# Kernel tuning notes

Measured on AMD Instinct MI355X. Metric: run time of the kernel, lower is better.

Reference implementation:

```python
import jax, jax.numpy as jnp
import numpy as np

B, T, C, L = 128, 1024, 128, 128
EPS = 1e-7        # keras.backend.epsilon()
NEG = -1e30       # log-space -inf surrogate


def setup_inputs() -> dict:
    key = jax.random.key(0)
    k1, k2, k3, k4 = jax.random.split(key, 4)
    logits = jax.random.normal(k1, (B, T, C), dtype=jnp.float32)
    y_pred = jax.nn.softmax(logits, axis=-1)                      # ctc_batch_cost expects probs
    y_true = jax.random.randint(k2, (B, L), 0, C - 1)             # blank = C-1 excluded from labels
    input_len = jax.random.randint(k3, (B, 1), T // 2, T + 1)
    label_len = jax.random.randint(k4, (B, 1), L // 2, L + 1)
    return {"y_true": y_true, "y_pred": y_pred, "input_len": input_len, "label_len": label_len}


def _ctc_loss(y_pred, y_true, input_len, label_len):
    # Faithful port of keras ctc_batch_cost: blank index = C-1, merge repeated,
    # log(y_pred + eps), returns per-sample loss with shape [B, 1].
    log_probs = jnp.log(y_pred + EPS)                             # [B,T,C]
    b, t_max, c = log_probs.shape
    blank = c - 1
    l = y_true.shape[1]
    s = 2 * l + 1
    # extended label sequence: blank, l1, blank, l2, ..., blank   [B,S]
    ext = jnp.full((b, s), blank, dtype=y_true.dtype).at[:, 1::2].set(y_true)
    # emission log-prob of each extended symbol at each frame     [B,T,S]
    lp_ext = jnp.take_along_axis(
        log_probs, jnp.broadcast_to(ext[:, None, :], (b, t_max, s)), axis=2)
    # skip transition s-2 -> s allowed iff ext[s] != blank and ext[s] != ext[s-2]
    allow_skip = jnp.concatenate(
        [jnp.zeros((b, 2), bool), (ext[:, 2:] != blank) & (ext[:, 2:] != ext[:, :-2])], axis=1)
    alpha0 = jnp.full((b, s), NEG, dtype=log_probs.dtype).at[:, 0].set(0.0)
    in_len = input_len.reshape(b, 1).astype(jnp.int32)

    def step(alpha, xt):
        lp_t, t = xt                                              # lp_t: [B,S]
        a1 = jnp.pad(alpha[:, :-1], ((0, 0), (1, 0)), constant_values=NEG)
        a2 = jnp.where(allow_skip,
                       jnp.pad(alpha[:, :-2], ((0, 0), (2, 0)), constant_values=NEG), NEG)
        new = lp_t + jnp.logaddexp(jnp.logaddexp(alpha, a1), a2)
        new = jnp.where(t < in_len, new, alpha)                   # freeze past input_len
        return new, None

    alpha, _ = jax.lax.scan(step, alpha0, (jnp.swapaxes(lp_ext, 0, 1), jnp.arange(t_max)))
    lab = label_len.reshape(b, 1).astype(jnp.int32)
    a_last = jnp.take_along_axis(alpha, 2 * lab, axis=1)          # ends at final blank
    a_prev = jnp.take_along_axis(alpha, jnp.maximum(2 * lab - 1, 0), axis=1)  # or final label
    return -jnp.logaddexp(a_last, a_prev)                         # [B,1]


def reference(y_true, y_pred, input_len, label_len):
    return _ctc_loss(y_pred, y_true, input_len, label_len)
```

## Files before the change

kernel.cpp:

```cpp
#include <hip/hip_runtime.h>
#include <cstdint>

#define NB 128
#define NT 1024
#define NC 128
#define NL 128
#define NS 257
#define EPSF 1e-7f
#define LN2F 0.69314718055994530942f
#define NEGL2 -1.442695e30f

__device__ __forceinline__ float fexp2(float x){ return __builtin_amdgcn_exp2f(x); }
__device__ __forceinline__ float flog2(float x){ return __builtin_amdgcn_logf(x); }

__device__ __forceinline__ float shup1(float x){
    int r = __builtin_amdgcn_update_dpp(0, __float_as_int(x), 0x138, 0xf, 0xf, true);
    return __int_as_float(r);
}
__device__ __forceinline__ int shup1i(int x){
    return __builtin_amdgcn_update_dpp(0, x, 0x138, 0xf, 0xf, true);
}

__device__ __forceinline__ void dma16(const float* g, float* lds){
    __builtin_amdgcn_global_load_lds((const __attribute__((address_space(1))) void*)g,
                                     (__attribute__((address_space(3))) void*)lds,
                                     16, 0, 0);
}

#define VM_DRAIN() asm volatile("s_waitcnt vmcnt(0)" ::: "memory")

#define FENCE12(S) asm volatile("" \
  : "+v"(S##B[0]),"+v"(S##B[1]),"+v"(S##B[2]),"+v"(S##B[3]), \
    "+v"(S##A[0]),"+v"(S##A[1]),"+v"(S##A[2]),"+v"(S##A[3]), \
    "+v"(S##C[0]),"+v"(S##C[1]),"+v"(S##C[2]),"+v"(S##C[3]))

#define FILL(S, gg) do{ _Pragma("unroll") \
    for (int r_ = 0; r_ < 4; ++r_){ \
        S##B[r_] = lB[((gg)*4 + r_) * NC]; \
        S##A[r_] = lA[((gg)*4 + r_) * NC]; \
        S##C[r_] = lC[((gg)*4 + r_) * NC]; } }while(0)

#define GROUP(S, gg) do{ _Pragma("unroll") \
    for (int r_ = 0; r_ < 4; ++r_){ \
        const bool commit_ = !freeze || ((k*32 + (gg)*4 + r_) < Tn); \
        step1(S##B[r_], S##A[r_], S##C[r_], commit_); \
        if (r_ < 3) shm3 = shup1(m3); } \
    boundary(early); }while(0)

__global__ __launch_bounds__(64,1)
void ctc_fwd_kernel(const int* __restrict__ y_true,
                    const float* __restrict__ y_pred,
                    const int* __restrict__ input_len,
                    const int* __restrict__ label_len,
                    float* __restrict__ out)
{
    __shared__ float buf[2][32 * NC];
    __shared__ float lg_alpha[NS + 3];

    const int b    = blockIdx.x;
    const int lane = threadIdx.x;
    const float* __restrict__ base = y_pred + (size_t)b * NT * NC;

    int Tn = input_len[b];
    Tn = Tn < 0 ? 0 : (Tn > NT ? NT : Tn);

    const int* __restrict__ yrow = y_true + b * NL;
    const int y0v = yrow[2 * lane]     & (NC - 1);
    const int y1v = yrow[2 * lane + 1] & (NC - 1);
    const int yp  = shup1i(y1v);
    const bool skip1 = (lane > 0) && (y0v != yp);
    const bool skip3 = (y1v != y0v);
    const bool isl0  = (lane == 0);
    const bool isl63 = (lane == 63);

    float m0 = isl0 ? 1.f : 0.f, m1 = 0.f, m2 = 0.f, m3 = 0.f, m4 = 0.f;
    float e   = 0.f;
    float f0  = isl0 ? 0.f : 1.f;
    float fs1 = skip1 ? f0 : 0.f;
    float shm3 = 0.f;

    float s0B[4], s0A[4], s0C[4], s1B[4], s1A[4], s1C[4];

    auto dma_chunk = [&](int c){
        const float* gsrc = base + (size_t)c * 32 * NC;
        float* dst = &buf[c & 1][0];
        #pragma unroll
        for (int i = 0; i < 16; ++i)
            dma16(gsrc + i * 256 + lane * 4, dst + i * 256);
    };

    auto step1 = [&](float Pb, float Pa, float Pc, bool commit){
        Pb += EPSF; Pa += EPSF; Pc += EPSF;
        float t3  = skip3 ? m1 : 0.f;
        float n3  = Pc * ((m3 + m2) + t3);
        float n2  = Pb * (m2 + m1);
        float n4  = Pb * (m4 + m3);
        float pm1 = shm3 * f0;
        float t1  = shm3 * fs1;
        float n0  = Pb * (m0 + pm1);
        float n1  = Pa * ((m1 + m0) + t1);
        if (commit) { m0 = n0; m1 = n1; m2 = n2; m3 = n3; m4 = n4; }
    };

    auto boundary = [&](bool early){
        float mx = fmaxf(fmaxf(m0, m1), fmaxf(m2, m3));
        if (isl63) mx = fmaxf(mx, m4);
        const uint32_t bx = __float_as_uint(mx);
        const uint32_t eb = bx >> 23;
        const float inv = __uint_as_float((254u - eb) << 23);
        const float ef  = (float)((int)eb - 127);
        const bool dead = (mx == 0.f);
        if (early) {
            float e1 = dead ? e : (e + ef);
            float s1 = shup1(e1);
            float e2 = (dead && !isl0) ? s1 : e1;
            float s2 = shup1(e2);
            e = (dead && !isl0) ? s2 : e2;
            float d = fminf(fmaxf(s2 - e, -126.f), 126.f);
            f0 = isl0 ? 0.f : fexp2(d);
        } else {
            e = dead ? e : (e + ef);
            float s1 = shup1(e);
            float d = fminf(fmaxf(s1 - e, -126.f), 126.f);
            f0 = isl0 ? 0.f : fexp2(d);
        }
        fs1 = skip1 ? f0 : 0.f;
        m0 *= inv; m1 *= inv; m2 *= inv; m3 *= inv; m4 *= inv;
        shm3 = shup1(m3);
    };

    auto chunkbody = [&](int k, bool early, bool freeze){
        const int h = k & 1;
        const float* lB = &buf[h][NC - 1];
        const float* lA = &buf[h][y0v];
        const float* lC = &buf[h][y1v];

        FILL(s0, 0);
        if (k + 1 < 32) dma_chunk(k + 1);

        FILL(s1, 1); FENCE12(s0); GROUP(s0, 0);
        FILL(s0, 2); FENCE12(s1); GROUP(s1, 1);
        FILL(s1, 3); FENCE12(s0); GROUP(s0, 2);
        FILL(s0, 4); FENCE12(s1); GROUP(s1, 3);
        FILL(s1, 5); FENCE12(s0); GROUP(s0, 4);
        FILL(s0, 6); FENCE12(s1); GROUP(s1, 5);
        FILL(s1, 7); FENCE12(s0); GROUP(s0, 6);
                     FENCE12(s1); GROUP(s1, 7);

        VM_DRAIN();
    };

    dma_chunk(0);
    VM_DRAIN();

    #pragma unroll 1
    for (int k = 0; k < 8; ++k)   chunkbody(k, true,  false);
    #pragma unroll 1
    for (int k = 8; k < 16; ++k)  chunkbody(k, false, false);
    #pragma unroll 1
    for (int k = 16; k < 32; ++k) chunkbody(k, false, true);

    lg_alpha[4 * lane + 0] = (m0 > 0.f) ? (e + flog2(m0)) : NEGL2;
    lg_alpha[4 * lane + 1] = (m1 > 0.f) ? (e + flog2(m1)) : NEGL2;
    lg_alpha[4 * lane + 2] = (m2 > 0.f) ? (e + flog2(m2)) : NEGL2;
    lg_alpha[4 * lane + 3] = (m3 > 0.f) ? (e + flog2(m3)) : NEGL2;
    if (isl63) lg_alpha[256] = (m4 > 0.f) ? (e + flog2(m4)) : NEGL2;
    __syncthreads();

    if (lane == 0) {
        int lab = label_len[b];
        lab = lab < 0 ? 0 : (lab > NL ? NL : lab);
        const int i_last = 2 * lab;
        const int i_prev = i_last > 0 ? i_last - 1 : 0;
        float A  = lg_alpha[i_last];
        float Bv = lg_alpha[i_prev];
        float mx = fmaxf(A, Bv);
        float r;
        if (mx < -1.0e29f) {
            r = mx;
        } else {
            float s = fexp2(A - mx) + fexp2(Bv - mx);
            r = mx + flog2(s);
        }
        out[b] = -r * LN2F;
    }
}

extern "C" void kernel_launch(void* const* d_in, const int* in_sizes, int n_in,
                              void* d_out, int out_size, void* d_ws, size_t ws_size,
                              hipStream_t stream) {
    const int*   y_true    = (const int*)d_in[0];
    const float* y_pred    = (const float*)d_in[1];
    const int*   input_len = (const int*)d_in[2];
    const int*   label_len = (const int*)d_in[3];
    float* outp = (float*)d_out;
    ctc_fwd_kernel<<<dim3(NB), dim3(64), 0, stream>>>(y_true, y_pred, input_len, label_len, outp);
}
```

Before: 156.4 us.

## Interleave two batch sequences per wavefront to expose instruction-level parallelism

Each block now processes two CTC sequences in one wavefront, interleaving their alpha recurrences, DMA loads and rescaling steps. The intent is to hide the dependency latency of the serial per-timestep recurrence by giving the scheduler two independent chains. In exchange the grid is halved, so fewer CUs are used and each wave does twice the serial work, and LDS and register use double.

```diff
diff --git a/kernel.cpp b/kernel.cpp
--- a/kernel.cpp
+++ b/kernel.cpp
@@ -2,6 +2,7 @@
 #include <cstdint>
 
 #define NB 128
+#define NBAT 2
 #define NT 1024
 #define NC 128
 #define NL 128
@@ -29,23 +30,75 @@
 
 #define VM_DRAIN() asm volatile("s_waitcnt vmcnt(0)" ::: "memory")
 
-#define FENCE12(S) asm volatile("" \
-  : "+v"(S##B[0]),"+v"(S##B[1]),"+v"(S##B[2]),"+v"(S##B[3]), \
-    "+v"(S##A[0]),"+v"(S##A[1]),"+v"(S##A[2]),"+v"(S##A[3]), \
-    "+v"(S##C[0]),"+v"(S##C[1]),"+v"(S##C[2]),"+v"(S##C[3]))
-
-#define FILL(S, gg) do{ _Pragma("unroll") \
-    for (int r_ = 0; r_ < 4; ++r_){ \
-        S##B[r_] = lB[((gg)*4 + r_) * NC]; \
-        S##A[r_] = lA[((gg)*4 + r_) * NC]; \
-        S##C[r_] = lC[((gg)*4 + r_) * NC]; } }while(0)
-
-#define GROUP(S, gg) do{ _Pragma("unroll") \
-    for (int r_ = 0; r_ < 4; ++r_){ \
-        const bool commit_ = !freeze || ((k*32 + (gg)*4 + r_) < Tn); \
-        step1(S##B[r_], S##A[r_], S##C[r_], commit_); \
-        if (r_ < 3) shm3 = shup1(m3); } \
-    boundary(early); }while(0)
+#define FENCE12(S, bi) asm volatile("" \
+  : "+v"(S##B[bi][0]),"+v"(S##B[bi][1]),"+v"(S##B[bi][2]),"+v"(S##B[bi][3]), \
+    "+v"(S##A[bi][0]),"+v"(S##A[bi][1]),"+v"(S##A[bi][2]),"+v"(S##A[bi][3]), \
+    "+v"(S##C[bi][0]),"+v"(S##C[bi][1]),"+v"(S##C[bi][2]),"+v"(S##C[bi][3]))
+
+#define FENCEALL(S) do{ _Pragma("unroll") \
+    for (int b_ = 0; b_ < NBAT; ++b_) FENCE12(S, b_); }while(0)
+
+#define FILLALL(S, gg) do{ _Pragma("unroll") \
+  for (int b_ = 0; b_ < NBAT; ++b_){ \
+    _Pragma("unroll") \
+    for (int r_ = 0; r_ < 4; ++r_) S##B[b_][r_] = lB[b_][((gg)*4 + r_) * NC]; \
+    _Pragma("unroll") \
+    for (int r_ = 0; r_ < 4; ++r_) S##A[b_][r_] = lA[b_][((gg)*4 + r_) * NC]; \
+    _Pragma("unroll") \
+    for (int r_ = 0; r_ < 4; ++r_) S##C[b_][r_] = lC[b_][((gg)*4 + r_) * NC]; \
+  } }while(0)
+
+#define STEP1(S, bi, gg, rr) do{ \
+    float Pb_ = S##B[bi][rr] + EPSF; \
+    float Pa_ = S##A[bi][rr] + EPSF; \
+    float Pc_ = S##C[bi][rr] + EPSF; \
+    float t3_ = skip3[bi] ? m1[bi] : 0.f; \
+    float n3_ = Pc_ * ((m3[bi] + m2[bi]) + t3_); \
+    float n2_ = Pb_ * (m2[bi] + m1[bi]); \
+    float n4_ = Pb_ * (m4[bi] + m3[bi]); \
+    float pm1_ = shm3[bi] * f0[bi]; \
+    float t1_ = shm3[bi] * fs1[bi]; \
+    float n0_ = Pb_ * (m0[bi] + pm1_); \
+    float n1_ = Pa_ * ((m1[bi] + m0[bi]) + t1_); \
+    const bool commit_ = !freeze || ((k*32 + (gg)*4 + (rr)) < Tn[bi]); \
+    if (commit_) { m0[bi]=n0_; m1[bi]=n1_; m2[bi]=n2_; m3[bi]=n3_; m4[bi]=n4_; } \
+  }while(0)
+
+#define BOUNDARY(bi) do{ \
+    float mx_ = fmaxf(fmaxf(m0[bi], m1[bi]), fmaxf(m2[bi], m3[bi])); \
+    if (isl63) mx_ = fmaxf(mx_, m4[bi]); \
+    const uint32_t bx_ = __float_as_uint(mx_); \
+    const uint32_t eb_ = bx_ >> 23; \
+    const float inv_ = __uint_as_float((254u - eb_) << 23); \
+    const float ef_  = (float)((int)eb_ - 127); \
+    const bool dead_ = (mx_ == 0.f); \
+    if (early) { \
+        float e1_ = dead_ ? e[bi] : (e[bi] + ef_); \
+        float s1_ = shup1(e1_); \
+        float e2_ = (dead_ && !isl0) ? s1_ : e1_; \
+        float s2_ = shup1(e2_); \
+        e[bi] = (dead_ && !isl0) ? s2_ : e2_; \
+        float d_ = fminf(fmaxf(s2_ - e[bi], -126.f), 126.f); \
+        f0[bi] = isl0 ? 0.f : fexp2(d_); \
+    } else { \
+        e[bi] = dead_ ? e[bi] : (e[bi] + ef_); \
+        float s1_ = shup1(e[bi]); \
+        float d_ = fminf(fmaxf(s1_ - e[bi], -126.f), 126.f); \
+        f0[bi] = isl0 ? 0.f : fexp2(d_); \
+    } \
+    fs1[bi] = skip1[bi] ? f0[bi] : 0.f; \
+    m0[bi] *= inv_; m1[bi] *= inv_; m2[bi] *= inv_; m3[bi] *= inv_; m4[bi] *= inv_; \
+    shm3[bi] = shup1(m3[bi]); \
+  }while(0)
+
+#define GROUPALL(S, gg) do{ _Pragma("unroll") \
+    for (int r_ = 0; r_ < 4; ++r_){ _Pragma("unroll") \
+      for (int b_ = 0; b_ < NBAT; ++b_){ \
+        STEP1(S, b_, gg, r_); \
+        if (r_ < 3) shm3[b_] = shup1(m3[b_]); } } \
+    _Pragma("unroll") \
+    for (int b_ = 0; b_ < NBAT; ++b_) BOUNDARY(b_); \
+  }while(0)
 
 __global__ __launch_bounds__(64,1)
 void ctc_fwd_kernel(const int* __restrict__ y_true,
@@ -54,126 +107,106 @@
                     const int* __restrict__ label_len,
                     float* __restrict__ out)
 {
-    __shared__ float buf[2][32 * NC];
-    __shared__ float lg_alpha[NS + 3];
-
-    const int b    = blockIdx.x;
+    __shared__ float buf[NBAT][2][32 * NC];
+    __shared__ float lg_alpha[NBAT][NS + 3];
+
+    const int b0   = blockIdx.x * NBAT;
     const int lane = threadIdx.x;
-    const float* __restrict__ base = y_pred + (size_t)b * NT * NC;
-
-    int Tn = input_len[b];
-    Tn = Tn < 0 ? 0 : (Tn > NT ? NT : Tn);
-
-    const int* __restrict__ yrow = y_true + b * NL;
-    const int y0v = yrow[2 * lane]     & (NC - 1);
-    const int y1v = yrow[2 * lane + 1] & (NC - 1);
-    const int yp  = shup1i(y1v);
-    const bool skip1 = (lane > 0) && (y0v != yp);
-    const bool skip3 = (y1v != y0v);
     const bool isl0  = (lane == 0);
     const bool isl63 = (lane == 63);
 
-    float m0 = isl0 ? 1.f : 0.f, m1 = 0.f, m2 = 0.f, m3 = 0.f, m4 = 0.f;
-    float e   = 0.f;
-    float f0  = isl0 ? 0.f : 1.f;
-    float fs1 = skip1 ? f0 : 0.f;
-    float shm3 = 0.f;
-
-    float s0B[4], s0A[4], s0C[4], s1B[4], s1A[4], s1C[4];
-
-    auto dma_chunk = [&](int c){
-        const float* gsrc = base + (size_t)c * 32 * NC;
-        float* dst = &buf[c & 1][0];
-        #pragma unroll
-        for (int i = 0; i < 16; ++i)
-            dma16(gsrc + i * 256 + lane * 4, dst + i * 256);
-    };
-
-    auto step1 = [&](float Pb, float Pa, float Pc, bool commit){
-        Pb += EPSF; Pa += EPSF; Pc += EPSF;
-        float t3  = skip3 ? m1 : 0.f;
-        float n3  = Pc * ((m3 + m2) + t3);
-        float n2  = Pb * (m2 + m1);
-        float n4  = Pb * (m4 + m3);
-        float pm1 = shm3 * f0;
-        float t1  = shm3 * fs1;
-        float n0  = Pb * (m0 + pm1);
-        float n1  = Pa * ((m1 + m0) + t1);
-        if (commit) { m0 = n0; m1 = n1; m2 = n2; m3 = n3; m4 = n4; }
-    };
-
-    auto boundary = [&](bool early){
-        float mx = fmaxf(fmaxf(m0, m1), fmaxf(m2, m3));
-        if (isl63) mx = fmaxf(mx, m4);
-        const uint32_t bx = __float_as_uint(mx);
-        const uint32_t eb = bx >> 23;
-        const float inv = __uint_as_float((254u - eb) << 23);
-        const float ef  = (float)((int)eb - 127);
-        const bool dead = (mx == 0.f);
-        if (early) {
-            float e1 = dead ? e : (e + ef);
-            float s1 = shup1(e1);
-            float e2 = (dead && !isl0) ? s1 : e1;
-            float s2 = shup1(e2);
-            e = (dead && !isl0) ? s2 : e2;
-            float d = fminf(fmaxf(s2 - e, -126.f), 126.f);
-            f0 = isl0 ? 0.f : fexp2(d);
-        } else {
-            e = dead ? e : (e + ef);
-            float s1 = shup1(e);
-            float d = fminf(fmaxf(s1 - e, -126.f), 126.f);
-            f0 = isl0 ? 0.f : fexp2(d);
+    const float* base[NBAT];
+    int   Tn[NBAT];
+    int   y0v[NBAT], y1v[NBAT];
+    bool  skip1[NBAT], skip3[NBAT];
+    float m0[NBAT], m1[NBAT], m2[NBAT], m3[NBAT], m4[NBAT];
+    float e[NBAT], f0[NBAT], fs1[NBAT], shm3[NBAT];
+    float s0B[NBAT][4], s0A[NBAT][4], s0C[NBAT][4];
+    float s1B[NBAT][4], s1A[NBAT][4], s1C[NBAT][4];
+
+#pragma unroll
+    for (int bi = 0; bi < NBAT; ++bi){
+        const int b = b0 + bi;
+        base[bi] = y_pred + (size_t)b * NT * NC;
+        int t = input_len[b];
+        Tn[bi] = t < 0 ? 0 : (t > NT ? NT : t);
+        const int* yrow = y_true + b * NL;
+        y0v[bi] = yrow[2 * lane]     & (NC - 1);
+        y1v[bi] = yrow[2 * lane + 1] & (NC - 1);
+        const int yp = shup1i(y1v[bi]);
+        skip1[bi] = (lane > 0) && (y0v[bi] != yp);
+        skip3[bi] = (y1v[bi] != y0v[bi]);
+        m0[bi] = isl0 ? 1.f : 0.f;
+        m1[bi] = m2[bi] = m3[bi] = m4[bi] = 0.f;
+        e[bi]  = 0.f;
+        f0[bi] = isl0 ? 0.f : 1.f;
+        fs1[bi] = skip1[bi] ? f0[bi] : 0.f;
+        shm3[bi] = 0.f;
+    }
+
+    auto dma_chunk_all = [&](int c){
+#pragma unroll
+        for (int bi = 0; bi < NBAT; ++bi){
+            const float* gsrc = base[bi] + (size_t)c * 32 * NC;
+            float* dst = &buf[bi][c & 1][0];
+#pragma unroll
+            for (int i = 0; i < 16; ++i)
+                dma16(gsrc + i * 256 + lane * 4, dst + i * 256);
         }
-        fs1 = skip1 ? f0 : 0.f;
-        m0 *= inv; m1 *= inv; m2 *= inv; m3 *= inv; m4 *= inv;
-        shm3 = shup1(m3);
     };
 
     auto chunkbody = [&](int k, bool early, bool freeze){
         const int h = k & 1;
-        const float* lB = &buf[h][NC - 1];
-        const float* lA = &buf[h][y0v];
-        const float* lC = &buf[h][y1v];
-
-        FILL(s0, 0);
-        if (k + 1 < 32) dma_chunk(k + 1);
-
-        FILL(s1, 1); FENCE12(s0); GROUP(s0, 0);
-        FILL(s0, 2); FENCE12(s1); GROUP(s1, 1);
-        FILL(s1, 3); FENCE12(s0); GROUP(s0, 2);
-        FILL(s0, 4); FENCE12(s1); GROUP(s1, 3);
-        FILL(s1, 5); FENCE12(s0); GROUP(s0, 4);
-        FILL(s0, 6); FENCE12(s1); GROUP(s1, 5);
-        FILL(s1, 7); FENCE12(s0); GROUP(s0, 6);
-                     FENCE12(s1); GROUP(s1, 7);
+        const float* lB[NBAT]; const float* lA[NBAT]; const float* lC[NBAT];
+#pragma unroll
+        for (int bi = 0; bi < NBAT; ++bi){
+            lB[bi] = &buf[bi][h][NC - 1];
+            lA[bi] = &buf[bi][h][y0v[bi]];
+            lC[bi] = &buf[bi][h][y1v[bi]];
+        }
+        FILLALL(s0, 0);
+        if (k + 1 < 32) dma_chunk_all(k + 1);
+
+        FILLALL(s1, 1); FENCEALL(s0); GROUPALL(s0, 0);
+        FILLALL(s0, 2); FENCEALL(s1); GROUPALL(s1, 1);
+        FILLALL(s1, 3); FENCEALL(s0); GROUPALL(s0, 2);
+        FILLALL(s0, 4); FENCEALL(s1); GROUPALL(s1, 3);
+        FILLALL(s1, 5); FENCEALL(s0); GROUPALL(s0, 4);
+        FILLALL(s0, 6); FENCEALL(s1); GROUPALL(s1, 5);
+        FILLALL(s1, 7); FENCEALL(s0); GROUPALL(s0, 6);
+                        FENCEALL(s1); GROUPALL(s1, 7);
 
         VM_DRAIN();
     };
 
-    dma_chunk(0);
+    dma_chunk_all(0);
     VM_DRAIN();
 
-    #pragma unroll 1
+#pragma unroll 1
     for (int k = 0; k < 8; ++k)   chunkbody(k, true,  false);
-    #pragma unroll 1
+#pragma unroll 1
     for (int k = 8; k < 16; ++k)  chunkbody(k, false, false);
-    #pragma unroll 1
+#pragma unroll 1
     for (int k = 16; k < 32; ++k) chunkbody(k, false, true);
 
-    lg_alpha[4 * lane + 0] = (m0 > 0.f) ? (e + flog2(m0)) : NEGL2;
-    lg_alpha[4 * lane + 1] = (m1 > 0.f) ? (e + flog2(m1)) : NEGL2;
-    lg_alpha[4 * lane + 2] = (m2 > 0.f) ? (e + flog2(m2)) : NEGL2;
-    lg_alpha[4 * lane + 3] = (m3 > 0.f) ? (e + flog2(m3)) : NEGL2;
-    if (isl63) lg_alpha[256] = (m4 > 0.f) ? (e + flog2(m4)) : NEGL2;
+#pragma unroll
+    for (int bi = 0; bi < NBAT; ++bi){
+        lg_alpha[bi][4 * lane + 0] = (m0[bi] > 0.f) ? (e[bi] + flog2(m0[bi])) : NEGL2;
+        lg_alpha[bi][4 * lane + 1] = (m1[bi] > 0.f) ? (e[bi] + flog2(m1[bi])) : NEGL2;
+        lg_alpha[bi][4 * lane + 2] = (m2[bi] > 0.f) ? (e[bi] + flog2(m2[bi])) : NEGL2;
+        lg_alpha[bi][4 * lane + 3] = (m3[bi] > 0.f) ? (e[bi] + flog2(m3[bi])) : NEGL2;
+        if (isl63) lg_alpha[bi][256] = (m4[bi] > 0.f) ? (e[bi] + flog2(m4[bi])) : NEGL2;
+    }
     __syncthreads();
 
-    if (lane == 0) {
-        int lab = label_len[b];
+    if (lane < NBAT) {
+        const int bi = lane;
+        int lab = label_len[b0 + bi];
         lab = lab < 0 ? 0 : (lab > NL ? NL : lab);
         const int i_last = 2 * lab;
         const int i_prev = i_last > 0 ? i_last - 1 : 0;
-        float A  = lg_alpha[i_last];
-        float Bv = lg_alpha[i_prev];
+        float A  = lg_alpha[bi][i_last];
+        float Bv = lg_alpha[bi][i_prev];
         float mx = fmaxf(A, Bv);
         float r;
         if (mx < -1.0e29f) {
@@ -182,7 +215,7 @@
             float s = fexp2(A - mx) + fexp2(Bv - mx);
             r = mx + flog2(s);
         }
-        out[b] = -r * LN2F;
+        out[b0 + bi] = -r * LN2F;
     }
 }
 
@@ -194,5 +227,5 @@
     const int*   input_len = (const int*)d_in[2];
     const int*   label_len = (const int*)d_in[3];
     float* outp = (float*)d_out;
-    ctc_fwd_kernel<<<dim3(NB), dim3(64), 0, stream>>>(y_true, y_pred, input_len, label_len, outp);
-}
+    ctc_fwd_kernel<<<dim3(NB / NBAT), dim3(64), 0, stream>>>(y_true, y_pred, input_len, label_len, outp);
+}
```

Measured after the change: 206.1 us. 1.32x slower.

## Use paired LDS reads with triple-buffered register prefetch and explicit lgkmcnt waits

Applied to the files above, without the earlier changes.

Replaces the per-element scalar LDS loads of emission probabilities with inline-asm ds_read2st64_b32 instructions that fetch two frames per read, halving LDS instruction count. The prefetch ring grows from two to three register sets with explicit s_waitcnt lgkmcnt counters, keeping two groups of reads in flight while the serial recurrence runs. This targets LDS latency on the per-timestep critical path. In exchange it adds register pressure and hand-managed wait counts that must stay correct, since the asm bypasses compiler tracking.

```diff
diff --git a/kernel.cpp b/kernel.cpp
--- a/kernel.cpp
+++ b/kernel.cpp
@@ -10,6 +10,8 @@
 #define LN2F 0.69314718055994530942f
 #define NEGL2 -1.442695e30f
 
+typedef float __attribute__((ext_vector_type(2))) v2f;
+
 __device__ __forceinline__ float fexp2(float x){ return __builtin_amdgcn_exp2f(x); }
 __device__ __forceinline__ float flog2(float x){ return __builtin_amdgcn_logf(x); }
 
@@ -29,21 +31,24 @@
 
 #define VM_DRAIN() asm volatile("s_waitcnt vmcnt(0)" ::: "memory")
 
-#define FENCE12(S) asm volatile("" \
-  : "+v"(S##B[0]),"+v"(S##B[1]),"+v"(S##B[2]),"+v"(S##B[3]), \
-    "+v"(S##A[0]),"+v"(S##A[1]),"+v"(S##A[2]),"+v"(S##A[3]), \
-    "+v"(S##C[0]),"+v"(S##C[1]),"+v"(S##C[2]),"+v"(S##C[3]))
-
-#define FILL(S, gg) do{ _Pragma("unroll") \
-    for (int r_ = 0; r_ < 4; ++r_){ \
-        S##B[r_] = lB[((gg)*4 + r_) * NC]; \
-        S##A[r_] = lA[((gg)*4 + r_) * NC]; \
-        S##C[r_] = lC[((gg)*4 + r_) * NC]; } }while(0)
+#define AS3U(p) ((unsigned)(size_t)(__attribute__((address_space(3))) void*)(p))
+
+#define WAITLGKM(N) do{ asm volatile("s_waitcnt lgkmcnt(" #N ")" ::: "memory"); \
+                        __builtin_amdgcn_sched_barrier(0); }while(0)
+
+#define FILLA(S, O0,O1,O2,O3) do{ \
+  asm volatile("ds_read2st64_b32 %0, %1 offset0:" #O0 " offset1:" #O1 : "=v"(S##B2[0]) : "v"(aB)); \
+  asm volatile("ds_read2st64_b32 %0, %1 offset0:" #O2 " offset1:" #O3 : "=v"(S##B2[1]) : "v"(aB)); \
+  asm volatile("ds_read2st64_b32 %0, %1 offset0:" #O0 " offset1:" #O1 : "=v"(S##A2[0]) : "v"(aA)); \
+  asm volatile("ds_read2st64_b32 %0, %1 offset0:" #O2 " offset1:" #O3 : "=v"(S##A2[1]) : "v"(aA)); \
+  asm volatile("ds_read2st64_b32 %0, %1 offset0:" #O0 " offset1:" #O1 : "=v"(S##C2[0]) : "v"(aC)); \
+  asm volatile("ds_read2st64_b32 %0, %1 offset0:" #O2 " offset1:" #O3 : "=v"(S##C2[1]) : "v"(aC)); \
+}while(0)
 
 #define GROUP(S, gg) do{ _Pragma("unroll") \
     for (int r_ = 0; r_ < 4; ++r_){ \
         const bool commit_ = !freeze || ((k*32 + (gg)*4 + r_) < Tn); \
-        step1(S##B[r_], S##A[r_], S##C[r_], commit_); \
+        step1(S##B2[r_>>1][r_&1], S##A2[r_>>1][r_&1], S##C2[r_>>1][r_&1], commit_); \
         if (r_ < 3) shm3 = shup1(m3); } \
     boundary(early); }while(0)
 
@@ -79,7 +84,9 @@
     float fs1 = skip1 ? f0 : 0.f;
     float shm3 = 0.f;
 
-    float s0B[4], s0A[4], s0C[4], s1B[4], s1A[4], s1C[4];
+    v2f s0B2[2], s0A2[2], s0C2[2];
+    v2f s1B2[2], s1A2[2], s1C2[2];
+    v2f s2B2[2], s2A2[2], s2C2[2];
 
     auto dma_chunk = [&](int c){
         const float* gsrc = base + (size_t)c * 32 * NC;
@@ -131,21 +138,22 @@
 
     auto chunkbody = [&](int k, bool early, bool freeze){
         const int h = k & 1;
-        const float* lB = &buf[h][NC - 1];
-        const float* lA = &buf[h][y0v];
-        const float* lC = &buf[h][y1v];
-
-        FILL(s0, 0);
+        const unsigned aB = AS3U(&buf[h][NC - 1]);
+        const unsigned aA = AS3U(&buf[h][y0v]);
+        const unsigned aC = AS3U(&buf[h][y1v]);
+
+        FILLA(s0,  0, 2, 4, 6);
         if (k + 1 < 32) dma_chunk(k + 1);
-
-        FILL(s1, 1); FENCE12(s0); GROUP(s0, 0);
-        FILL(s0, 2); FENCE12(s1); GROUP(s1, 1);
-        FILL(s1, 3); FENCE12(s0); GROUP(s0, 2);
-        FILL(s0, 4); FENCE12(s1); GROUP(s1, 3);
-        FILL(s1, 5); FENCE12(s0); GROUP(s0, 4);
-        FILL(s0, 6); FENCE12(s1); GROUP(s1, 5);
-        FILL(s1, 7); FENCE12(s0); GROUP(s0, 6);
-                     FENCE12(s1); GROUP(s1, 7);
+        FILLA(s1,  8,10,12,14);
+
+        FILLA(s2, 16,18,20,22); WAITLGKM(12); GROUP(s0, 0);
+        FILLA(s0, 24,26,28,30); WAITLGKM(12); GROUP(s1, 1);
+        FILLA(s1, 32,34,36,38); WAITLGKM(12); GROUP(s2, 2);
+        FILLA(s2, 40,42,44,46); WAITLGKM(12); GROUP(s0, 3);
+        FILLA(s0, 48,50,52,54); WAITLGKM(12); GROUP(s1, 4);
+        FILLA(s1, 56,58,60,62); WAITLGKM(12); GROUP(s2, 5);
+                                WAITLGKM(6);  GROUP(s0, 6);
+                                WAITLGKM(0);  GROUP(s1, 7);
 
         VM_DRAIN();
     };
```

Measured after the change: 147.2 us. 1.06x faster.
